# Optimization experiments

Measured on AMD Instinct MI355X. Metric: run time of the kernel, lower is better.

## Reference

```python
import jax, jax.numpy as jnp
import numpy as np

ROWS, COLS, N_CHARS = 384, 768, 69  # CHARSET length = 69
CH, CW = 28, 14  # char tile height, width


def setup_inputs() -> dict:
    key = jax.random.key(0)
    k1, k2 = jax.random.split(key)
    grid_logits = jax.random.normal(k1, (ROWS, COLS, N_CHARS), dtype=jnp.float32)
    # font rasterizations are in [0, 1] (pixel intensity / 255)
    font = jax.random.uniform(k2, (N_CHARS, CH, CW), dtype=jnp.float32)
    return {"grid_logits": grid_logits, "font": font}


def reference(grid_logits, font):
    rows, cols, n_chars = grid_logits.shape
    ch, cw = font.shape[1], font.shape[2]
    # softmax over characters per grid cell
    probs = jax.nn.softmax(grid_logits, axis=-1)  # (R, C, N)
    # soft blend of font tiles: (R, C, ch, cw)
    soft_tiles = jnp.einsum('rcn,nhw->rchw', probs, font)
    # assemble full image: equivalent to nested torch.cat over rows/cols
    soft_image = soft_tiles.transpose(0, 2, 1, 3).reshape(rows * ch, cols * cw)
    return soft_image[None, None]  # (1, 1, H, W)
```

## Files before the change

### kernel.cpp

```cpp
#include <hip/hip_runtime.h>
#include <hip/hip_bf16.h>

#define ROWS 384
#define COLS 768
#define NCH  69
#define CH   28
#define CW   14
#define KP   96
#define IMG_W 10752
#define ROW_U 104

typedef __attribute__((ext_vector_type(8))) short bfrag;
typedef __attribute__((ext_vector_type(4))) float f32x4;

__device__ __forceinline__ unsigned bf16bits(float x) {
    unsigned b = __float_as_uint(x);
    b += 0x7FFFu + ((b >> 16) & 1u);
    return b >> 16;
}

__global__ __launch_bounds__(256)
void font_prep(const float* __restrict__ font, unsigned short* __restrict__ Fh) {
    int idx = blockIdx.x * 256 + threadIdx.x;
    if (idx >= CH * 16 * KP) return;
    int k  = idx % KP;
    int hw = idx / KP;
    int w  = hw % 16, h = hw / 16;
    float v = (w < CW && k < NCH) ? font[k * (CH * CW) + h * CW + w] : 0.f;
    Fh[idx] = (unsigned short)bf16bits(v);
}

__global__ __launch_bounds__(128, 3)
void diffrender_v6(const float* __restrict__ logits,
                   const unsigned short* __restrict__ Fh,
                   float* __restrict__ out)
{
    __shared__ __align__(16) unsigned short smem[2][64 * ROW_U];

    const int tid  = threadIdx.x;
    const int lane = tid & 63;
    const int wv   = tid >> 6;
    const int cell = blockIdx.x * 128 + tid;
    const int r    = blockIdx.x / 6;
    const int cb   = (blockIdx.x % 6) * 128;

    const float* lp = logits + (size_t)cell * NCH;
    float e[NCH];
    float m = -INFINITY;
#pragma unroll
    for (int n = 0; n < NCH; ++n) { e[n] = lp[n]; m = fmaxf(m, e[n]); }
    float s = 0.f;
#pragma unroll
    for (int n = 0; n < NCH; ++n) { e[n] = __expf(e[n] - m); s += e[n]; }
    const float inv = 1.f / s;

    unsigned* prow = (unsigned*)&smem[wv][(size_t)lane * ROW_U];
#pragma unroll
    for (int i = 0; i < 34; ++i)
        prow[i] = bf16bits(e[2 * i] * inv) | (bf16bits(e[2 * i + 1] * inv) << 16);
    prow[34] = bf16bits(e[68] * inv);
#pragma unroll
    for (int i = 35; i < 48; ++i) prow[i] = 0;

    const int w15   = lane & 15;
    const int kgrp  = (lane >> 4) * 8;
    const int crow4 = (lane >> 4) * 4;
    bfrag a[4][3];
#pragma unroll
    for (int mt = 0; mt < 4; ++mt)
#pragma unroll
        for (int ks = 0; ks < 3; ++ks)
            a[mt][ks] = *(const bfrag*)&smem[wv][(size_t)(mt * 16 + w15) * ROW_U + ks * 32 + kgrp];

    float* stage = (float*)&smem[wv][0];

    const unsigned short* fb = Fh + (size_t)w15 * KP + kgrp;
    bfrag bcur[2][3], bnxt[2][3];
#pragma unroll
    for (int hh = 0; hh < 2; ++hh)
#pragma unroll
        for (int ks = 0; ks < 3; ++ks)
            bcur[hh][ks] = *(const bfrag*)(fb + (size_t)(hh * 16) * KP + ks * 32);

#pragma unroll 1
    for (int h2 = 0; h2 < CH / 2; ++h2) {
        const int h = 2 * h2;
        if (h2 + 1 < CH / 2) {
            const unsigned short* fn = fb + (size_t)((h + 2) * 16) * KP;
#pragma unroll
            for (int hh = 0; hh < 2; ++hh)
#pragma unroll
                for (int ks = 0; ks < 3; ++ks)
                    bnxt[hh][ks] = *(const bfrag*)(fn + (size_t)(hh * 16) * KP + ks * 32);
        }

        f32x4 acc[2][4];
#pragma unroll
        for (int hh = 0; hh < 2; ++hh)
#pragma unroll
            for (int mt = 0; mt < 4; ++mt)
                acc[hh][mt] = f32x4{0, 0, 0, 0};
#pragma unroll
        for (int hh = 0; hh < 2; ++hh)
#pragma unroll
            for (int mt = 0; mt < 4; ++mt)
#pragma unroll
                for (int ks = 0; ks < 3; ++ks)
                    acc[hh][mt] = __builtin_amdgcn_mfma_f32_16x16x32_bf16(
                        a[mt][ks], bcur[hh][ks], acc[hh][mt], 0, 0, 0);

        if (w15 < CW) {
#pragma unroll
            for (int hh = 0; hh < 2; ++hh)
#pragma unroll
                for (int mt = 0; mt < 4; ++mt)
#pragma unroll
                    for (int j = 0; j < 4; ++j)
                        stage[hh * 896 + (mt * 16 + crow4 + j) * CW + w15] = acc[hh][mt][j];
        }

#pragma unroll
        for (int hh = 0; hh < 2; ++hh) {
            float4* o4 = (float4*)(out + (size_t)(r * CH + h + hh) * IMG_W
                                       + (size_t)(cb + wv * 64) * CW);
            const float4* s4 = (const float4*)(stage + hh * 896);
#pragma unroll
            for (int i = 0; i < 4; ++i) {
                const int idx = i * 64 + lane;
                if (idx < 224) o4[idx] = s4[idx];
            }
        }

#pragma unroll
        for (int hh = 0; hh < 2; ++hh)
#pragma unroll
            for (int ks = 0; ks < 3; ++ks)
                bcur[hh][ks] = bnxt[hh][ks];
    }
}

extern "C" void kernel_launch(void* const* d_in, const int* in_sizes, int n_in,
                              void* d_out, int out_size, void* d_ws, size_t ws_size,
                              hipStream_t stream) {
    const float* logits = (const float*)d_in[0];
    const float* font   = (const float*)d_in[1];
    float* out          = (float*)d_out;
    unsigned short* Fh  = (unsigned short*)d_ws;

    font_prep<<<(CH * 16 * KP + 255) / 256, 256, 0, stream>>>(font, Fh);

    const int blocks = (ROWS * COLS) / 128;
    diffrender_v6<<<blocks, 128, 0, stream>>>(logits, Fh, out);
}
```

Before: 122.0 us.

## Stage logits into LDS with coalesced direct global-to-LDS loads, one wave per block

```diff
diff --git a/kernel.cpp b/kernel.cpp
--- a/kernel.cpp
+++ b/kernel.cpp
@@ -9,6 +9,7 @@
 #define KP   96
 #define IMG_W 10752
 #define ROW_U 104
+#define CHUNK_B (64 * NCH * 4)
 
 typedef __attribute__((ext_vector_type(8))) short bfrag;
 typedef __attribute__((ext_vector_type(4))) float f32x4;
@@ -17,6 +18,12 @@
     unsigned b = __float_as_uint(x);
     b += 0x7FFFu + ((b >> 16) & 1u);
     return b >> 16;
+}
+
+__device__ __forceinline__ void gload_lds16(const void* g, void* l) {
+    __builtin_amdgcn_global_load_lds(
+        (const __attribute__((address_space(1))) void*)g,
+        (__attribute__((address_space(3))) void*)l, 16, 0, 0);
 }
 
 __global__ __launch_bounds__(256)
@@ -30,31 +37,37 @@
     Fh[idx] = (unsigned short)bf16bits(v);
 }
 
-__global__ __launch_bounds__(128, 3)
-void diffrender_v6(const float* __restrict__ logits,
+__global__ __launch_bounds__(64, 2)
+void diffrender_v7(const float* __restrict__ logits,
                    const unsigned short* __restrict__ Fh,
                    float* __restrict__ out)
 {
-    __shared__ __align__(16) unsigned short smem[2][64 * ROW_U];
+    __shared__ __align__(16) unsigned char smem[CHUNK_B];
 
-    const int tid  = threadIdx.x;
-    const int lane = tid & 63;
-    const int wv   = tid >> 6;
-    const int cell = blockIdx.x * 128 + tid;
-    const int r    = blockIdx.x / 6;
-    const int cb   = (blockIdx.x % 6) * 128;
+    const int lane = threadIdx.x;
+    const int bid  = blockIdx.x;
+    const int r    = bid / 12;
+    const int cb   = (bid % 12) * 64;
 
-    const float* lp = logits + (size_t)cell * NCH;
+    const char* gbase = (const char*)logits + (size_t)bid * CHUNK_B;
+#pragma unroll
+    for (int i = 0; i < 18; ++i) {
+        const int off = (i < 17) ? i * 1024 : (CHUNK_B - 1024);
+        gload_lds16(gbase + off + lane * 16, (void*)(smem + off));
+    }
+    asm volatile("s_waitcnt vmcnt(0)" ::: "memory");
+
+    const float* myrow = (const float*)smem + (size_t)lane * NCH;
     float e[NCH];
     float m = -INFINITY;
 #pragma unroll
-    for (int n = 0; n < NCH; ++n) { e[n] = lp[n]; m = fmaxf(m, e[n]); }
+    for (int n = 0; n < NCH; ++n) { e[n] = myrow[n]; m = fmaxf(m, e[n]); }
     float s = 0.f;
 #pragma unroll
     for (int n = 0; n < NCH; ++n) { e[n] = __expf(e[n] - m); s += e[n]; }
     const float inv = 1.f / s;
 
-    unsigned* prow = (unsigned*)&smem[wv][(size_t)lane * ROW_U];
+    unsigned* prow = (unsigned*)(smem + (size_t)lane * (ROW_U * 2));
 #pragma unroll
     for (int i = 0; i < 34; ++i)
         prow[i] = bf16bits(e[2 * i] * inv) | (bf16bits(e[2 * i + 1] * inv) << 16);
@@ -65,14 +78,15 @@
     const int w15   = lane & 15;
     const int kgrp  = (lane >> 4) * 8;
     const int crow4 = (lane >> 4) * 4;
+    const unsigned short* pa = (const unsigned short*)smem;
     bfrag a[4][3];
 #pragma unroll
     for (int mt = 0; mt < 4; ++mt)
 #pragma unroll
         for (int ks = 0; ks < 3; ++ks)
-            a[mt][ks] = *(const bfrag*)&smem[wv][(size_t)(mt * 16 + w15) * ROW_U + ks * 32 + kgrp];
+            a[mt][ks] = *(const bfrag*)&pa[(size_t)(mt * 16 + w15) * ROW_U + ks * 32 + kgrp];
 
-    float* stage = (float*)&smem[wv][0];
+    float* stage = (float*)smem;
 
     const unsigned short* fb = Fh + (size_t)w15 * KP + kgrp;
     bfrag bcur[2][3], bnxt[2][3];
@@ -122,7 +136,7 @@
 #pragma unroll
         for (int hh = 0; hh < 2; ++hh) {
             float4* o4 = (float4*)(out + (size_t)(r * CH + h + hh) * IMG_W
-                                       + (size_t)(cb + wv * 64) * CW);
+                                       + (size_t)cb * CW);
             const float4* s4 = (const float4*)(stage + hh * 896);
 #pragma unroll
             for (int i = 0; i < 4; ++i) {
@@ -149,6 +163,6 @@
 
     font_prep<<<(CH * 16 * KP + 255) / 256, 256, 0, stream>>>(font, Fh);
 
-    const int blocks = (ROWS * COLS) / 128;
-    diffrender_v6<<<blocks, 128, 0, stream>>>(logits, Fh, out);
+    const int blocks = (ROWS * COLS) / 64;
+    diffrender_v7<<<blocks, 64, 0, stream>>>(logits, Fh, out);
 }
```

New measurement: 122.1 us. No clear change (+0.1%).
